# Kernel optimization log

Hardware: AMD Instinct MI355X
Metric: run time of the kernel (lower is better)

Reference implementation:

```python
import jax, jax.numpy as jnp
import numpy as np

EMB = 1024
HEADS = 16
DH = EMB // HEADS
EPS = 1e-5


def _layernorm(x, w, b):
    mean = jnp.mean(x, axis=-1, keepdims=True)
    var = jnp.mean((x - mean) ** 2, axis=-1, keepdims=True)  # unbiased=False
    return w * (x - mean) / jnp.sqrt(var + EPS) + b


def _gelu_tanh(x):
    c = jnp.sqrt(jnp.asarray(2.0 / jnp.pi, x.dtype))
    return 0.5 * x * (1.0 + jnp.tanh(c * (x + 0.044715 * x ** 3)))


def setup_inputs() -> dict:
    key = jax.random.key(0)
    ks = jax.random.split(key, 8)
    B, N = 2, 2048
    s = lambda fan_in: 1.0 / np.sqrt(fan_in)
    # weights stored as [in, out] (torch Linear applied as x @ W.T == x @ W_here)
    return {
        "x": jax.random.normal(ks[0], (B, N, EMB), jnp.float32),
        "ln1_w": jnp.ones((EMB,), jnp.float32),
        "ln1_b": jnp.zeros((EMB,), jnp.float32),
        "w_qkv": jax.random.normal(ks[1], (EMB, 3 * EMB), jnp.float32) * s(EMB),  # qkv_bias=False
        "w_attn_proj": jax.random.normal(ks[2], (EMB, EMB), jnp.float32) * s(EMB),
        "b_attn_proj": jnp.zeros((EMB,), jnp.float32),
        "ln2_w": jnp.ones((EMB,), jnp.float32),
        "ln2_b": jnp.zeros((EMB,), jnp.float32),
        "w_fc": jax.random.normal(ks[3], (EMB, 4 * EMB), jnp.float32) * s(EMB),
        "b_fc": jnp.zeros((4 * EMB,), jnp.float32),
        "w_proj": jax.random.normal(ks[4], (4 * EMB, EMB), jnp.float32) * s(4 * EMB),
        "b_proj": jnp.zeros((EMB,), jnp.float32),
    }


def reference(x, ln1_w, ln1_b, w_qkv, w_attn_proj, b_attn_proj,
              ln2_w, ln2_b, w_fc, b_fc, w_proj, b_proj):
    B, N, _ = x.shape
    # --- attention sublayer (pre-LN) ---
    h = _layernorm(x, ln1_w, ln1_b)
    qkv = h @ w_qkv  # [B,N,3E]
    q, k, v = jnp.split(qkv, 3, axis=-1)
    # [B,H,N,Dh]
    q = q.reshape(B, N, HEADS, DH).transpose(0, 2, 1, 3)
    k = k.reshape(B, N, HEADS, DH).transpose(0, 2, 1, 3)
    v = v.reshape(B, N, HEADS, DH).transpose(0, 2, 1, 3)
    scores = jnp.einsum("bhqd,bhkd->bhqk", q, k) * (DH ** -0.5)
    causal = jnp.tril(jnp.ones((N, N), bool))
    scores = jnp.where(causal, scores, -jnp.inf)
    attn = jax.nn.softmax(scores, axis=-1)  # attn_pdrop=0 (eval)
    ctx = jnp.einsum("bhqk,bhkd->bhqd", attn, v)
    ctx = ctx.transpose(0, 2, 1, 3).reshape(B, N, EMB)
    x = x + (ctx @ w_attn_proj + b_attn_proj)  # resid_pdrop=0
    # --- MLP sublayer (pre-LN) ---
    h = _layernorm(x, ln2_w, ln2_b)
    h = _gelu_tanh(h @ w_fc + b_fc)
    x = x + (h @ w_proj + b_proj)
    return x
```

## Files before the change

### kernel.cpp

```cpp
#include <hip/hip_runtime.h>
#include <stdint.h>

#define EMB 1024
#define NHEAD 16
#define DH 64
#define SEQ 2048
#define NTOK 4096

typedef __attribute__((ext_vector_type(8))) short s16x8;
typedef __attribute__((ext_vector_type(4))) short s16x4;
typedef __attribute__((ext_vector_type(4))) float f32x4;
typedef __attribute__((ext_vector_type(4))) unsigned short u16x4;

__device__ __forceinline__ unsigned short f2bf(float f){
    union { float f; unsigned int u; } v; v.f = f;
    unsigned int r = v.u + 0x7fffu + ((v.u >> 16) & 1u);
    return (unsigned short)(r >> 16);
}

__device__ __forceinline__ f32x4 mfma16(s16x8 a, s16x8 b, f32x4 c){
    return __builtin_amdgcn_mfma_f32_16x16x32_bf16(a, b, c, 0, 0, 0);
}

__device__ __forceinline__ void gload16(const void* g, void* l){
    __builtin_amdgcn_global_load_lds((const __attribute__((address_space(1))) void*)g,
                                     (__attribute__((address_space(3))) void*)l, 16, 0, 0);
}

__device__ __forceinline__ s16x8 cat8(s16x4 a, s16x4 b){
    s16x8 r;
    r[0]=a[0]; r[1]=a[1]; r[2]=a[2]; r[3]=a[3];
    r[4]=b[0]; r[5]=b[1]; r[6]=b[2]; r[7]=b[3];
    return r;
}

__device__ __forceinline__ unsigned cvtpk(float lo, float hi){
    unsigned r;
    asm("v_cvt_pk_bf16_f32 %0, %1, %2" : "=v"(r) : "v"(lo), "v"(hi));
    return r;
}

__device__ __forceinline__ s16x8 qscale(s16x8 q){
    s16x8 r;
    #pragma unroll
    for (int e = 0; e < 8; ++e){
        union { float f; unsigned u; } v;
        v.u = ((unsigned)(unsigned short)q[e]) << 16;
        v.f *= 0.125f;
        r[e] = (short)f2bf(v.f);
    }
    return r;
}

__global__ __launch_bounds__(256) void convT4_kernel(const float* __restrict__ q, unsigned short* __restrict__ qo,
                                                     const float* __restrict__ a, unsigned short* __restrict__ ao,
                                                     const float* __restrict__ f, unsigned short* __restrict__ fo,
                                                     const float* __restrict__ p, unsigned short* __restrict__ po){
    __shared__ float tile[32][33];
    int id = blockIdx.x;
    const float* in; unsigned short* out; int R, C, bx, by;
    if (id < 3072)      { in = q; out = qo; R = 1024; C = 3072; bx = id % 96;  by = id / 96;  }
    else if (id < 4096) { id -= 3072; in = a; out = ao; R = 1024; C = 1024; bx = id % 32; by = id / 32; }
    else if (id < 8192) { id -= 4096; in = f; out = fo; R = 1024; C = 4096; bx = id % 128; by = id / 128; }
    else                { id -= 8192; in = p; out = po; R = 4096; C = 1024; bx = id % 32; by = id / 32; }
    const int c0 = bx * 32, r0 = by * 32;
    const int tx = threadIdx.x, ty = threadIdx.y;
    #pragma unroll
    for (int k = 0; k < 4; ++k)
        tile[ty*4+k][tx] = in[(long)(r0 + ty*4 + k) * C + c0 + tx];
    __syncthreads();
    #pragma unroll
    for (int k = 0; k < 4; ++k)
        out[(long)(c0 + ty*4 + k) * R + r0 + tx] = f2bf(tile[tx][ty*4+k]);
}

__global__ __launch_bounds__(256) void vT_kernel(const unsigned short* __restrict__ qkv,
                                                 unsigned short* __restrict__ vtg){
    __shared__ unsigned short tile[64*64];
    const int bh = blockIdx.y, b = bh >> 4, h = bh & 15;
    const int n0 = blockIdx.x * 64;
    const int t = threadIdx.x;
    const int nr = t >> 3, c0 = (t & 7) * 8;
    #pragma unroll
    for (int hh = 0; hh < 2; ++hh){
        const int n = nr + hh*32;
        uint4 vv = *(const uint4*)&qkv[(long)(b*SEQ + n0 + n)*3072 + 2048 + h*64 + c0];
        *(uint4*)((char*)tile + n*128 + ((c0*2) ^ (((n>>3)&7)<<4))) = vv;
    }
    __syncthreads();
    #pragma unroll
    for (int hh = 0; hh < 2; ++hh){
        const int d = nr + hh*32;
        union { unsigned short u[8]; uint4 v; } tmp;
        #pragma unroll
        for (int j = 0; j < 8; ++j){
            const int n = c0 + j;
            tmp.u[j] = *(const unsigned short*)((char*)tile + n*128 + ((d*2) ^ (((n>>3)&7)<<4)));
        }
        *(uint4*)&vtg[((long)bh*64 + d)*2048 + n0 + c0] = tmp.v;
    }
}

__global__ __launch_bounds__(256) void ln_kernel(const float* __restrict__ x,
                                                 const float* __restrict__ w,
                                                 const float* __restrict__ b,
                                                 unsigned short* __restrict__ out){
    const int row = blockIdx.x, tid = threadIdx.x;
    const float4 v = ((const float4*)(x + (long)row * EMB))[tid];
    float s  = v.x + v.y + v.z + v.w;
    float ss = v.x*v.x + v.y*v.y + v.z*v.z + v.w*v.w;
    #pragma unroll
    for (int off = 32; off >= 1; off >>= 1){
        s  += __shfl_xor(s,  off, 64);
        ss += __shfl_xor(ss, off, 64);
    }
    __shared__ float ps[4], pss[4];
    const int wv = tid >> 6;
    if ((tid & 63) == 0){ ps[wv] = s; pss[wv] = ss; }
    __syncthreads();
    s  = ps[0] + ps[1] + ps[2] + ps[3];
    ss = pss[0] + pss[1] + pss[2] + pss[3];
    const float mean = s * (1.0f/EMB);
    const float var  = ss * (1.0f/EMB) - mean*mean;
    const float rstd = rsqrtf(var + 1e-5f);
    const float4 wv4 = ((const float4*)w)[tid];
    const float4 bv4 = ((const float4*)b)[tid];
    u16x4 o;
    o[0] = f2bf((v.x - mean) * rstd * wv4.x + bv4.x);
    o[1] = f2bf((v.y - mean) * rstd * wv4.y + bv4.y);
    o[2] = f2bf((v.z - mean) * rstd * wv4.z + bv4.z);
    o[3] = f2bf((v.w - mean) * rstd * wv4.w + bv4.w);
    *(u16x4*)(out + (long)row * EMB + tid * 4) = o;
}

__global__ __launch_bounds__(256) void red_kernel(const float* __restrict__ p0,
                                                  const float* __restrict__ p1,
                                                  const float* __restrict__ bias,
                                                  const float* __restrict__ resid,
                                                  float* __restrict__ out, int N){
    const long i = ((long)blockIdx.x * 256 + threadIdx.x) * 4;
    const float4 a = *(const float4*)(p0 + i);
    const float4 b = *(const float4*)(p1 + i);
    const float4 r = *(const float4*)(resid + i);
    const float4 bb = *(const float4*)(bias + ((int)i & (N - 1)));
    float4 o;
    o.x = a.x + b.x + r.x + bb.x;
    o.y = a.y + b.y + r.y + bb.y;
    o.z = a.z + b.z + r.z + bb.z;
    o.w = a.w + b.w + r.w + bb.w;
    *(float4*)(out + i) = o;
}

template<int EPI, int SK>
__global__ __launch_bounds__(256, 2) void gemm4_kernel(const unsigned short* __restrict__ A,
                                                       const unsigned short* __restrict__ Bt,
                                                       const float* __restrict__ bias,
                                                       void* __restrict__ out0,
                                                       void* __restrict__ out1,
                                                       int M, int N, int K){
    __shared__ unsigned short As[2][128*64];
    __shared__ unsigned short Bs[2][128*64];
    const int tid = threadIdx.x, lane = tid & 63, w = tid >> 6;
    const int lm = lane & 15, g = lane >> 4;
    const int wr = w >> 1, wc = w & 1;

    const int gx = gridDim.x;
    const int nwg = gx * gridDim.y;
    int id = blockIdx.y * gx + blockIdx.x;
    id = (id & 7) * (nwg >> 3) + (id >> 3);
    const int m0 = (id / gx) * 128, n0 = (id % gx) * 128;
    const int kz = (SK > 1) ? blockIdx.z : 0;
    const int kbase = kz * (K / SK);
    const int nkt = (K / SK) / 64;

    const int r8 = tid >> 3;
    const int src = (((tid & 7) * 16) ^ ((r8 & 7) << 4)) >> 1;
    char* AsB = (char*)&As[0][0];
    char* BsB = (char*)&Bs[0][0];

    auto stage = [&](int bu, int kt){
        #pragma unroll
        for (int p = 0; p < 4; ++p)
            gload16(&A[(long)(m0 + p*32 + r8) * K + kt + src], AsB + bu*16384 + p*4096 + tid*16);
        #pragma unroll
        for (int p = 0; p < 4; ++p)
            gload16(&Bt[(long)(n0 + p*32 + r8) * K + kt + src], BsB + bu*16384 + p*4096 + tid*16);
    };

    f32x4 zero = {0.0f, 0.0f, 0.0f, 0.0f};
    f32x4 acc[4][4];
    #pragma unroll
    for (int i = 0; i < 4; ++i)
        #pragma unroll
        for (int j = 0; j < 4; ++j) acc[i][j] = zero;

    stage(0, kbase);
    int cur = 0;
    const int axor = (lm & 7) << 4;
    for (int t = 0; t < nkt; ++t){
        if (t + 1 < nkt){
            stage(cur ^ 1, kbase + (t + 1) * 64);
            asm volatile("s_waitcnt vmcnt(8)" ::: "memory");
        } else {
            asm volatile("s_waitcnt vmcnt(0)" ::: "memory");
        }
        __builtin_amdgcn_s_barrier();
        asm volatile("" ::: "memory");
        const char* Ab = AsB + cur*16384;
        const char* Bb = BsB + cur*16384;
        #pragma unroll
        for (int kk = 0; kk < 2; ++kk){
            s16x8 af[4], bf[4];
            #pragma unroll
            for (int i = 0; i < 4; ++i)
                af[i] = *(const s16x8*)(Ab + (wr*64 + i*16 + lm)*128 + ((kk*64 + g*16) ^ axor));
            #pragma unroll
            for (int j = 0; j < 4; ++j)
                bf[j] = *(const s16x8*)(Bb + (wc*64 + j*16 + lm)*128 + ((kk*64 + g*16) ^ axor));
            asm volatile("s_waitcnt lgkmcnt(0)" ::: "memory");
            __builtin_amdgcn_sched_barrier(0);
            __builtin_amdgcn_s_setprio(1);
            #pragma unroll
            for (int i = 0; i < 4; ++i)
                #pragma unroll
                for (int j = 0; j < 4; ++j)
                    acc[i][j] = mfma16(af[i], bf[j], acc[i][j]);
            __builtin_amdgcn_s_setprio(0);
        }
        asm volatile("" ::: "memory");
        __builtin_amdgcn_s_barrier();
        asm volatile("" ::: "memory");
        cur ^= 1;
    }

    float* po = (SK > 1 && kz == 1) ? (float*)out1 : (float*)out0;
    #pragma unroll
    for (int i = 0; i < 4; ++i){
        #pragma unroll
        for (int r = 0; r < 4; ++r){
            const int row = m0 + wr*64 + i*16 + 4*g + r;
            #pragma unroll
            for (int j = 0; j < 4; ++j){
                const int col = n0 + wc*64 + j*16 + lm;
                const float v = acc[i][j][r];
                if (EPI == 0){
                    ((unsigned short*)out0)[(long)row * N + col] = f2bf(v);
                } else if (EPI == 2){
                    const float xx = v + bias[col];
                    const float z = 0.7978845608f * (xx + 0.044715f * xx * xx * xx);
                    const float gg = xx / (1.0f + __expf(-2.0f * z));
                    ((unsigned short*)out0)[(long)row * N + col] = f2bf(gg);
                } else {
                    po[(long)row * N + col] = v;
                }
            }
        }
    }
}

template<int EPI, int SK>
__global__ __launch_bounds__(256, 3) void gemm5_kernel(const unsigned short* __restrict__ A,
                                                       const unsigned short* __restrict__ Bt,
                                                       const float* __restrict__ bias,
                                                       const float* __restrict__ resid,
                                                       float* __restrict__ out0,
                                                       float* __restrict__ out1,
                                                       int M, int N, int K,
                                                       int xr, int yr){
    __shared__ unsigned short As[2][128*64];
    __shared__ unsigned short Bs[2][64*64];
    const int tid = threadIdx.x, lane = tid & 63, w = tid >> 6;
    const int lm = lane & 15, g = lane >> 4;
    const int wr = w >> 1, wc = w & 1;

    const int gx = gridDim.x;
    const int o = blockIdx.y * gx + blockIdx.x;
    const int x = o & 7, j = o >> 3;
    const int nrx = gx / xr;
    const int m0 = ((x / nrx) * yr + j / xr) * 128;
    const int n0 = ((x % nrx) * xr + j % xr) * 64;
    const int kz = (SK > 1) ? blockIdx.z : 0;
    const int kbase = kz * (K / SK);
    const int nkt = (K / SK) / 64;

    const int r8 = tid >> 3;
    const int src = (((tid & 7) * 16) ^ ((r8 & 7) << 4)) >> 1;
    char* AsB = (char*)&As[0][0];
    char* BsB = (char*)&Bs[0][0];

    auto stage = [&](int bu, int kt){
        #pragma unroll
        for (int p = 0; p < 4; ++p)
            gload16(&A[(long)(m0 + p*32 + r8) * K + kt + src], AsB + bu*16384 + p*4096 + tid*16);
        #pragma unroll
        for (int p = 0; p < 2; ++p)
            gload16(&Bt[(long)(n0 + p*32 + r8) * K + kt + src], BsB + bu*8192 + p*4096 + tid*16);
    };

    f32x4 zero = {0.0f, 0.0f, 0.0f, 0.0f};
    f32x4 acc[4][2];
    #pragma unroll
    for (int i = 0; i < 4; ++i)
        #pragma unroll
        for (int jj = 0; jj < 2; ++jj) acc[i][jj] = zero;

    stage(0, kbase);
    int cur = 0;
    const int axor = (lm & 7) << 4;
    for (int t = 0; t < nkt; ++t){
        if (t + 1 < nkt){
            stage(cur ^ 1, kbase + (t + 1) * 64);
            asm volatile("s_waitcnt vmcnt(6)" ::: "memory");
        } else {
            asm volatile("s_waitcnt vmcnt(0)" ::: "memory");
        }
        __builtin_amdgcn_s_barrier();
        asm volatile("" ::: "memory");
        const char* Ab = AsB + cur*16384;
        const char* Bb = BsB + cur*8192;
        #pragma unroll
        for (int kk = 0; kk < 2; ++kk){
            s16x8 af[4], bf[2];
            #pragma unroll
            for (int i = 0; i < 4; ++i)
                af[i] = *(const s16x8*)(Ab + (wr*64 + i*16 + lm)*128 + ((kk*64 + g*16) ^ axor));
            #pragma unroll
            for (int jj = 0; jj < 2; ++jj)
                bf[jj] = *(const s16x8*)(Bb + (wc*32 + jj*16 + lm)*128 + ((kk*64 + g*16) ^ axor));
            asm volatile("s_waitcnt lgkmcnt(0)" ::: "memory");
            __builtin_amdgcn_sched_barrier(0);
            __builtin_amdgcn_s_setprio(1);
            #pragma unroll
            for (int i = 0; i < 4; ++i)
                #pragma unroll
                for (int jj = 0; jj < 2; ++jj)
                    acc[i][jj] = mfma16(bf[jj], af[i], acc[i][jj]);
            __builtin_amdgcn_s_setprio(0);
        }
        asm volatile("" ::: "memory");
        __builtin_amdgcn_s_barrier();
        asm volatile("" ::: "memory");
        cur ^= 1;
    }

    float* po = (SK > 1 && kz == 1) ? out1 : out0;
    #pragma unroll
    for (int i = 0; i < 4; ++i){
        const int row = m0 + wr*64 + i*16 + lm;
        #pragma unroll
        for (int jj = 0; jj < 2; ++jj){
            const int col = n0 + wc*32 + jj*16 + 4*g;
            const f32x4 v = acc[i][jj];
            if (EPI == 1){
                const float4 bb = *(const float4*)&bias[col];
                const float4 rr = *(const float4*)&resid[(long)row * N + col];
                float4 ov;
                ov.x = v[0] + bb.x + rr.x;
                ov.y = v[1] + bb.y + rr.y;
                ov.z = v[2] + bb.z + rr.z;
                ov.w = v[3] + bb.w + rr.w;
                *(float4*)&out0[(long)row * N + col] = ov;
            } else {
                *(float4*)&po[(long)row * N + col] = *(const float4*)&v;
            }
        }
    }
}

template<int EPI, int BM, int BN, int WR, int WC, int SK>
__global__ __launch_bounds__(WR*WC*64) void gemm_kernel(const unsigned short* __restrict__ A,
                                                        const unsigned short* __restrict__ Bt,
                                                        const float* __restrict__ bias,
                                                        const float* __restrict__ resid,
                                                        void* __restrict__ out0,
                                                        void* __restrict__ out1,
                                                        int M, int N, int K){
    constexpr int NW = WR * WC;
    constexpr int NT = NW * 64;
    constexpr int FI = BM / (WR * 16);
    constexpr int FJ = BN / (WC * 16);
    __shared__ unsigned short As[2][BM * 32];
    __shared__ unsigned short Bs[2][BN * 32];
    const int tid  = threadIdx.x;
    const int lane = tid & 63, w = tid >> 6;
    const int lm = lane & 15, g = lane >> 4;
    const int wr = w / WC, wc = w % WC;

    const int gx = gridDim.x;
    const int nwg = gx * gridDim.y;
    int id = blockIdx.y * gx + blockIdx.x;
    id = (id & 7) * (nwg >> 3) + (id >> 3);
    const int m0 = (id / gx) * BM, n0 = (id % gx) * BN;
    const int kz = (SK > 1) ? blockIdx.z : 0;
    const int kbase = kz * (K / SK);

    f32x4 zero = {0.0f, 0.0f, 0.0f, 0.0f};
    f32x4 acc[FI][FJ];
    #pragma unroll
    for (int i = 0; i < FI; ++i)
        #pragma unroll
        for (int j = 0; j < FJ; ++j) acc[i][j] = zero;

    auto stage = [&](int kt, int bu){
        #pragma unroll
        for (int p = 0; p < BM/(NT/4); ++p)
            gload16(&A[(long)(m0 + p*(NT/4) + (tid>>2)) * K + kt + (tid&3)*8],
                    (char*)&As[bu][0] + p*(NT*16) + tid*16);
        #pragma unroll
        for (int p = 0; p < BN/(NT/4); ++p)
            gload16(&Bt[(long)(n0 + p*(NT/4) + (tid>>2)) * K + kt + (tid&3)*8],
                    (char*)&Bs[bu][0] + p*(NT*16) + tid*16);
    };

    stage(kbase, 0);
    int cur = 0;
    const int nkt = (K / SK) / 32;
    for (int t = 0; t < nkt; ++t){
        __syncthreads();
        if (t + 1 < nkt) stage(kbase + (t+1)*32, cur ^ 1);
        s16x8 af[FI], bf[FJ];
        #pragma unroll
        for (int i = 0; i < FI; ++i)
            af[i] = *(const s16x8*)&As[cur][(wr*(FI*16) + i*16 + lm)*32 + g*8];
        #pragma unroll
        for (int j = 0; j < FJ; ++j)
            bf[j] = *(const s16x8*)&Bs[cur][(wc*(FJ*16) + j*16 + lm)*32 + g*8];
        #pragma unroll
        for (int i = 0; i < FI; ++i)
            #pragma unroll
            for (int j = 0; j < FJ; ++j)
                acc[i][j] = mfma16(af[i], bf[j], acc[i][j]);
        cur ^= 1;
    }

    float* po = (SK > 1 && kz == 1) ? (float*)out1 : (float*)out0;
    #pragma unroll
    for (int i = 0; i < FI; ++i){
        #pragma unroll
        for (int r = 0; r < 4; ++r){
            const int row = m0 + wr*(FI*16) + i*16 + 4*g + r;
            #pragma unroll
            for (int j = 0; j < FJ; ++j){
                const int col = n0 + wc*(FJ*16) + j*16 + lm;
                const float v = acc[i][j][r];
                if (EPI == 0){
                    ((unsigned short*)out0)[(long)row * N + col] = f2bf(v);
                } else if (EPI == 1){
                    ((float*)out0)[(long)row * N + col] =
                        v + bias[col] + resid[(long)row * N + col];
                } else if (EPI == 2){
                    const float xx = v + bias[col];
                    const float z = 0.7978845608f * (xx + 0.044715f * xx * xx * xx);
                    const float gg = xx / (1.0f + __expf(-2.0f * z));
                    ((unsigned short*)out0)[(long)row * N + col] = f2bf(gg);
                } else {
                    po[(long)row * N + col] = v;
                }
            }
        }
    }
}

__global__ __launch_bounds__(256) void attn_kernel(const unsigned short* __restrict__ qkv,
                                                   const unsigned short* __restrict__ vtg,
                                                   unsigned short* __restrict__ ctx){
    __shared__ unsigned short Ks[3][4096];
    __shared__ unsigned short Vs[3][4096];
    int id0 = blockIdx.y * 16 + blockIdx.x;
    const int id = (id0 & 7) * 64 + (id0 >> 3);
    const int pair = id & 15, bh = id >> 4;
    const int b = bh >> 4, h = bh & 15;
    const int tid = threadIdx.x, lane = tid & 63, w = tid >> 6;
    const int lm = lane & 15, g = lane >> 4;
    const long qkvb = (long)b * SEQ * 3072;
    const unsigned short* kglob = qkv + qkvb + 1024 + h*64;
    const unsigned short* vglob = vtg + (long)bh * 64 * 2048;

    const int srow = tid >> 3;
    const int soff = (tid & 7) * 16;
    const int swz = (lm & 7) << 4;
    f32x4 zero = {0.0f, 0.0f, 0.0f, 0.0f};

    #pragma unroll 1
    for (int grp = 0; grp < 2; ++grp){
        const int qg = (grp == 0) ? pair : (31 - pair);
        const int q0 = qg * 64;
        const int nt = qg + 1;
        const int qrow = q0 + w*16 + lm;

        const unsigned short* qrp = qkv + qkvb + (long)qrow*3072 + h*64;
        const s16x8 qf0 = qscale(*(const s16x8*)(qrp + g*8));
        const s16x8 qf1 = qscale(*(const s16x8*)(qrp + 32 + g*8));

        f32x4 o[4];
        #pragma unroll
        for (int d = 0; d < 4; ++d) o[d] = zero;
        float lsum = 0.0f;

        auto stageKV = [&](int t, int bu){
            const int kv0 = t * 64;
            #pragma unroll
            for (int hh = 0; hh < 2; ++hh){
                const int row = srow + hh*32;
                const int sw  = soff ^ ((row & 7) << 4);
                gload16(kglob + (long)(kv0 + row)*3072 + (sw >> 1),
                        (char*)&Ks[bu][0] + hh*4096 + w*1024);
                gload16(vglob + (long)row*2048 + kv0 + (sw >> 1),
                        (char*)&Vs[bu][0] + hh*4096 + w*1024);
            }
        };
        auto qkt = [&](int bu, f32x4* sc){
            const char* Kb = (const char*)&Ks[bu][0];
            #pragma unroll
            for (int s = 0; s < 4; ++s){
                const char* rp = Kb + (s*16 + lm)*128;
                s16x8 kf0 = *(const s16x8*)(rp + ((g*16) ^ swz));
                s16x8 kf1 = *(const s16x8*)(rp + ((64 + g*16) ^ swz));
                f32x4 a = mfma16(kf0, qf0, zero);
                sc[s] = mfma16(kf1, qf1, a);
            }
        };

        __builtin_amdgcn_s_barrier();
        asm volatile("" ::: "memory");
        stageKV(0, 0);
        if (nt > 1){
            stageKV(1, 1);
            asm volatile("s_waitcnt vmcnt(4)" ::: "memory");
        } else {
            asm volatile("s_waitcnt vmcnt(0)" ::: "memory");
        }
        __builtin_amdgcn_s_barrier();
        asm volatile("" ::: "memory");

        f32x4 sc[4], scN[4];
        qkt(0, sc);

        #pragma unroll 1
        for (int t = 0; t < nt; ++t){
            const bool more = (t + 1 < nt);
            if (more){
                asm volatile("s_waitcnt vmcnt(0)" ::: "memory");
                __builtin_amdgcn_s_barrier();
                asm volatile("" ::: "memory");
                if (t + 2 < nt) stageKV(t + 2, (t + 2) % 3);
                qkt((t + 1) % 3, scN);
            }

            if (t == nt - 1){
                #pragma unroll
                for (int s = 0; s < 4; ++s)
                    #pragma unroll
                    for (int r = 0; r < 4; ++r)
                        if (s*16 + 4*g + r > w*16 + lm) sc[s][r] = -1e30f;
            }
            float pp[4][4];
            #pragma unroll
            for (int s = 0; s < 4; ++s)
                #pragma unroll
                for (int r = 0; r < 4; ++r){
                    const float e = __expf(sc[s][r]);
                    pp[s][r] = e;
                    lsum += e;
                }

            union { unsigned u[4]; s16x8 v; } P0, P1;
            P0.u[0] = cvtpk(pp[0][0], pp[0][1]);
            P0.u[1] = cvtpk(pp[0][2], pp[0][3]);
            P0.u[2] = cvtpk(pp[1][0], pp[1][1]);
            P0.u[3] = cvtpk(pp[1][2], pp[1][3]);
            P1.u[0] = cvtpk(pp[2][0], pp[2][1]);
            P1.u[1] = cvtpk(pp[2][2], pp[2][3]);
            P1.u[2] = cvtpk(pp[3][0], pp[3][1]);
            P1.u[3] = cvtpk(pp[3][2], pp[3][3]);

            const char* Vb = (const char*)&Vs[t % 3][0];
            #pragma unroll
            for (int d = 0; d < 4; ++d){
                const char* vrp = Vb + (d*16 + lm)*128;
                s16x4 a0 = *(const s16x4*)(vrp + ((g*8) ^ swz));
                s16x4 a1 = *(const s16x4*)(vrp + ((32 + g*8) ^ swz));
                o[d] = mfma16(cat8(a0, a1), P0.v, o[d]);
                s16x4 b0 = *(const s16x4*)(vrp + ((64 + g*8) ^ swz));
                s16x4 b1 = *(const s16x4*)(vrp + ((96 + g*8) ^ swz));
                o[d] = mfma16(cat8(b0, b1), P1.v, o[d]);
            }
            if (more){
                #pragma unroll
                for (int s4 = 0; s4 < 4; ++s4) sc[s4] = scN[s4];
            }
        }

        lsum += __shfl_xor(lsum, 16, 64);
        lsum += __shfl_xor(lsum, 32, 64);
        const float inv = 1.0f / lsum;
        unsigned short* cw = ctx + (long)(b*SEQ + qrow)*EMB + h*DH + 4*g;
        #pragma unroll
        for (int d = 0; d < 4; ++d){
            u16x4 ov;
            ov[0] = f2bf(o[d][0]*inv); ov[1] = f2bf(o[d][1]*inv);
            ov[2] = f2bf(o[d][2]*inv); ov[3] = f2bf(o[d][3]*inv);
            *(u16x4*)(cw + d*16) = ov;
        }
    }
}

extern "C" void kernel_launch(void* const* d_in, const int* in_sizes, int n_in,
                              void* d_out, int out_size, void* d_ws, size_t ws_size,
                              hipStream_t stream){
    const float* x     = (const float*)d_in[0];
    const float* ln1_w = (const float*)d_in[1];
    const float* ln1_b = (const float*)d_in[2];
    const float* w_qkv = (const float*)d_in[3];
    const float* w_ap  = (const float*)d_in[4];
    const float* b_ap  = (const float*)d_in[5];
    const float* ln2_w = (const float*)d_in[6];
    const float* ln2_b = (const float*)d_in[7];
    const float* w_fc  = (const float*)d_in[8];
    const float* b_fc  = (const float*)d_in[9];
    const float* w_pr  = (const float*)d_in[10];
    const float* b_pr  = (const float*)d_in[11];
    float* out = (float*)d_out;

    char* ws = (char*)d_ws;
    unsigned short* wqkvT = (unsigned short*)(ws + 0);
    unsigned short* wapT  = (unsigned short*)(ws + 6291456);
    unsigned short* wfcT  = (unsigned short*)(ws + 8388608);
    unsigned short* wprT  = (unsigned short*)(ws + 16777216);
    unsigned short* h1    = (unsigned short*)(ws + 25165824);
    unsigned short* vtg   = (unsigned short*)(ws + 25165824);
    unsigned short* qkv   = (unsigned short*)(ws + 33554432);
    unsigned short* ctx   = (unsigned short*)(ws + 58720256);
    float*          x1    = (float*)(ws + 67108864);
    unsigned short* h2    = (unsigned short*)(ws + 83886080);
    unsigned short* afc   = (unsigned short*)(ws + 92274688);
    float* pp0 = (float*)(ws + 0);
    float* pp1 = (float*)(ws + 25165824);

    convT4_kernel<<<12288, dim3(32, 8, 1), 0, stream>>>(
        w_qkv, wqkvT, w_ap, wapT, w_fc, wfcT, w_pr, wprT);

    ln_kernel<<<NTOK, 256, 0, stream>>>(x, ln1_w, ln1_b, h1);

    gemm4_kernel<0,1><<<dim3(3072/128, NTOK/128), 256, 0, stream>>>(
        h1, wqkvT, nullptr, qkv, nullptr, NTOK, 3072, 1024);

    vT_kernel<<<dim3(SEQ/64, 32), 256, 0, stream>>>(qkv, vtg);

    attn_kernel<<<dim3(16, 32), 256, 0, stream>>>(qkv, vtg, ctx);

    gemm_kernel<1,128,64,2,2,1><<<dim3(1024/64, NTOK/128), 256, 0, stream>>>(
        ctx, wapT, b_ap, x, x1, nullptr, NTOK, 1024, 1024);

    ln_kernel<<<NTOK, 256, 0, stream>>>(x1, ln2_w, ln2_b, h2);

    gemm4_kernel<2,1><<<dim3(4096/128, NTOK/128), 256, 0, stream>>>(
        h2, wfcT, b_fc, afc, nullptr, NTOK, 4096, 1024);

    gemm5_kernel<3,2><<<dim3(1024/64, NTOK/128, 2), 256, 0, stream>>>(
        afc, wprT, nullptr, nullptr, pp0, pp1, NTOK, 1024, 4096, 8, 8);
    red_kernel<<<NTOK*EMB/1024, 256, 0, stream>>>(pp0, pp1, b_pr, x1, out, EMB);
}
```

Before: 248.8 us.

## Drop split-K on MLP down-projection and fuse bias+residual into GEMM epilogue

```diff
diff --git a/kernel.cpp b/kernel.cpp
--- a/kernel.cpp
+++ b/kernel.cpp
@@ -133,30 +133,11 @@
     *(u16x4*)(out + (long)row * EMB + tid * 4) = o;
 }
 
-__global__ __launch_bounds__(256) void red_kernel(const float* __restrict__ p0,
-                                                  const float* __restrict__ p1,
-                                                  const float* __restrict__ bias,
-                                                  const float* __restrict__ resid,
-                                                  float* __restrict__ out, int N){
-    const long i = ((long)blockIdx.x * 256 + threadIdx.x) * 4;
-    const float4 a = *(const float4*)(p0 + i);
-    const float4 b = *(const float4*)(p1 + i);
-    const float4 r = *(const float4*)(resid + i);
-    const float4 bb = *(const float4*)(bias + ((int)i & (N - 1)));
-    float4 o;
-    o.x = a.x + b.x + r.x + bb.x;
-    o.y = a.y + b.y + r.y + bb.y;
-    o.z = a.z + b.z + r.z + bb.z;
-    o.w = a.w + b.w + r.w + bb.w;
-    *(float4*)(out + i) = o;
-}
-
-template<int EPI, int SK>
+template<int EPI>
 __global__ __launch_bounds__(256, 2) void gemm4_kernel(const unsigned short* __restrict__ A,
                                                        const unsigned short* __restrict__ Bt,
                                                        const float* __restrict__ bias,
                                                        void* __restrict__ out0,
-                                                       void* __restrict__ out1,
                                                        int M, int N, int K){
     __shared__ unsigned short As[2][128*64];
     __shared__ unsigned short Bs[2][128*64];
@@ -169,9 +150,7 @@
     int id = blockIdx.y * gx + blockIdx.x;
     id = (id & 7) * (nwg >> 3) + (id >> 3);
     const int m0 = (id / gx) * 128, n0 = (id % gx) * 128;
-    const int kz = (SK > 1) ? blockIdx.z : 0;
-    const int kbase = kz * (K / SK);
-    const int nkt = (K / SK) / 64;
+    const int nkt = K / 64;
 
     const int r8 = tid >> 3;
     const int src = (((tid & 7) * 16) ^ ((r8 & 7) << 4)) >> 1;
@@ -194,12 +173,12 @@
         #pragma unroll
         for (int j = 0; j < 4; ++j) acc[i][j] = zero;
 
-    stage(0, kbase);
+    stage(0, 0);
     int cur = 0;
     const int axor = (lm & 7) << 4;
     for (int t = 0; t < nkt; ++t){
         if (t + 1 < nkt){
-            stage(cur ^ 1, kbase + (t + 1) * 64);
+            stage(cur ^ 1, (t + 1) * 64);
             asm volatile("s_waitcnt vmcnt(8)" ::: "memory");
         } else {
             asm volatile("s_waitcnt vmcnt(0)" ::: "memory");
@@ -233,7 +212,6 @@
         cur ^= 1;
     }
 
-    float* po = (SK > 1 && kz == 1) ? (float*)out1 : (float*)out0;
     #pragma unroll
     for (int i = 0; i < 4; ++i){
         #pragma unroll
@@ -245,26 +223,22 @@
                 const float v = acc[i][j][r];
                 if (EPI == 0){
                     ((unsigned short*)out0)[(long)row * N + col] = f2bf(v);
-                } else if (EPI == 2){
+                } else {
                     const float xx = v + bias[col];
                     const float z = 0.7978845608f * (xx + 0.044715f * xx * xx * xx);
                     const float gg = xx / (1.0f + __expf(-2.0f * z));
                     ((unsigned short*)out0)[(long)row * N + col] = f2bf(gg);
-                } else {
-                    po[(long)row * N + col] = v;
                 }
             }
         }
     }
 }
 
-template<int EPI, int SK>
 __global__ __launch_bounds__(256, 3) void gemm5_kernel(const unsigned short* __restrict__ A,
                                                        const unsigned short* __restrict__ Bt,
                                                        const float* __restrict__ bias,
                                                        const float* __restrict__ resid,
                                                        float* __restrict__ out0,
-                                                       float* __restrict__ out1,
                                                        int M, int N, int K,
                                                        int xr, int yr){
     __shared__ unsigned short As[2][128*64];
@@ -279,9 +253,7 @@
     const int nrx = gx / xr;
     const int m0 = ((x / nrx) * yr + j / xr) * 128;
     const int n0 = ((x % nrx) * xr + j % xr) * 64;
-    const int kz = (SK > 1) ? blockIdx.z : 0;
-    const int kbase = kz * (K / SK);
-    const int nkt = (K / SK) / 64;
+    const int nkt = K / 64;
 
     const int r8 = tid >> 3;
     const int src = (((tid & 7) * 16) ^ ((r8 & 7) << 4)) >> 1;
@@ -304,12 +276,12 @@
         #pragma unroll
         for (int jj = 0; jj < 2; ++jj) acc[i][jj] = zero;
 
-    stage(0, kbase);
+    stage(0, 0);
     int cur = 0;
     const int axor = (lm & 7) << 4;
     for (int t = 0; t < nkt; ++t){
         if (t + 1 < nkt){
-            stage(cur ^ 1, kbase + (t + 1) * 64);
+            stage(cur ^ 1, (t + 1) * 64);
             asm volatile("s_waitcnt vmcnt(6)" ::: "memory");
         } else {
             asm volatile("s_waitcnt vmcnt(0)" ::: "memory");
@@ -343,7 +315,6 @@
         cur ^= 1;
     }
 
-    float* po = (SK > 1 && kz == 1) ? out1 : out0;
     #pragma unroll
     for (int i = 0; i < 4; ++i){
         const int row = m0 + wr*64 + i*16 + lm;
@@ -351,29 +322,24 @@
         for (int jj = 0; jj < 2; ++jj){
             const int col = n0 + wc*32 + jj*16 + 4*g;
             const f32x4 v = acc[i][jj];
-            if (EPI == 1){
-                const float4 bb = *(const float4*)&bias[col];
-                const float4 rr = *(const float4*)&resid[(long)row * N + col];
-                float4 ov;
-                ov.x = v[0] + bb.x + rr.x;
-                ov.y = v[1] + bb.y + rr.y;
-                ov.z = v[2] + bb.z + rr.z;
-                ov.w = v[3] + bb.w + rr.w;
-                *(float4*)&out0[(long)row * N + col] = ov;
-            } else {
-                *(float4*)&po[(long)row * N + col] = *(const float4*)&v;
-            }
-        }
-    }
-}
-
-template<int EPI, int BM, int BN, int WR, int WC, int SK>
+            const float4 bb = *(const float4*)&bias[col];
+            const float4 rr = *(const float4*)&resid[(long)row * N + col];
+            float4 ov;
+            ov.x = v[0] + bb.x + rr.x;
+            ov.y = v[1] + bb.y + rr.y;
+            ov.z = v[2] + bb.z + rr.z;
+            ov.w = v[3] + bb.w + rr.w;
+            *(float4*)&out0[(long)row * N + col] = ov;
+        }
+    }
+}
+
+template<int EPI, int BM, int BN, int WR, int WC>
 __global__ __launch_bounds__(WR*WC*64) void gemm_kernel(const unsigned short* __restrict__ A,
                                                         const unsigned short* __restrict__ Bt,
                                                         const float* __restrict__ bias,
                                                         const float* __restrict__ resid,
                                                         void* __restrict__ out0,
-                                                        void* __restrict__ out1,
                                                         int M, int N, int K){
     constexpr int NW = WR * WC;
     constexpr int NT = NW * 64;
@@ -391,8 +357,6 @@
     int id = blockIdx.y * gx + blockIdx.x;
     id = (id & 7) * (nwg >> 3) + (id >> 3);
     const int m0 = (id / gx) * BM, n0 = (id % gx) * BN;
-    const int kz = (SK > 1) ? blockIdx.z : 0;
-    const int kbase = kz * (K / SK);
 
     f32x4 zero = {0.0f, 0.0f, 0.0f, 0.0f};
     f32x4 acc[FI][FJ];
@@ -412,12 +376,12 @@
                     (char*)&Bs[bu][0] + p*(NT*16) + tid*16);
     };
 
-    stage(kbase, 0);
+    stage(0, 0);
     int cur = 0;
-    const int nkt = (K / SK) / 32;
+    const int nkt = K / 32;
     for (int t = 0; t < nkt; ++t){
         __syncthreads();
-        if (t + 1 < nkt) stage(kbase + (t+1)*32, cur ^ 1);
+        if (t + 1 < nkt) stage((t+1)*32, cur ^ 1);
         s16x8 af[FI], bf[FJ];
         #pragma unroll
         for (int i = 0; i < FI; ++i)
@@ -433,7 +397,6 @@
         cur ^= 1;
     }
 
-    float* po = (SK > 1 && kz == 1) ? (float*)out1 : (float*)out0;
     #pragma unroll
     for (int i = 0; i < FI; ++i){
         #pragma unroll
@@ -443,18 +406,11 @@
             for (int j = 0; j < FJ; ++j){
                 const int col = n0 + wc*(FJ*16) + j*16 + lm;
                 const float v = acc[i][j][r];
-                if (EPI == 0){
-                    ((unsigned short*)out0)[(long)row * N + col] = f2bf(v);
-                } else if (EPI == 1){
+                if (EPI == 1){
                     ((float*)out0)[(long)row * N + col] =
                         v + bias[col] + resid[(long)row * N + col];
-                } else if (EPI == 2){
-                    const float xx = v + bias[col];
-                    const float z = 0.7978845608f * (xx + 0.044715f * xx * xx * xx);
-                    const float gg = xx / (1.0f + __expf(-2.0f * z));
-                    ((unsigned short*)out0)[(long)row * N + col] = f2bf(gg);
                 } else {
-                    po[(long)row * N + col] = v;
+                    ((unsigned short*)out0)[(long)row * N + col] = f2bf(v);
                 }
             }
         }
@@ -634,30 +590,27 @@
     float*          x1    = (float*)(ws + 67108864);
     unsigned short* h2    = (unsigned short*)(ws + 83886080);
     unsigned short* afc   = (unsigned short*)(ws + 92274688);
-    float* pp0 = (float*)(ws + 0);
-    float* pp1 = (float*)(ws + 25165824);
 
     convT4_kernel<<<12288, dim3(32, 8, 1), 0, stream>>>(
         w_qkv, wqkvT, w_ap, wapT, w_fc, wfcT, w_pr, wprT);
 
     ln_kernel<<<NTOK, 256, 0, stream>>>(x, ln1_w, ln1_b, h1);
 
-    gemm4_kernel<0,1><<<dim3(3072/128, NTOK/128), 256, 0, stream>>>(
-        h1, wqkvT, nullptr, qkv, nullptr, NTOK, 3072, 1024);
+    gemm4_kernel<0><<<dim3(3072/128, NTOK/128), 256, 0, stream>>>(
+        h1, wqkvT, nullptr, qkv, NTOK, 3072, 1024);
 
     vT_kernel<<<dim3(SEQ/64, 32), 256, 0, stream>>>(qkv, vtg);
 
     attn_kernel<<<dim3(16, 32), 256, 0, stream>>>(qkv, vtg, ctx);
 
-    gemm_kernel<1,128,64,2,2,1><<<dim3(1024/64, NTOK/128), 256, 0, stream>>>(
-        ctx, wapT, b_ap, x, x1, nullptr, NTOK, 1024, 1024);
+    gemm_kernel<1,128,64,2,2><<<dim3(1024/64, NTOK/128), 256, 0, stream>>>(
+        ctx, wapT, b_ap, x, x1, NTOK, 1024, 1024);
 
     ln_kernel<<<NTOK, 256, 0, stream>>>(x1, ln2_w, ln2_b, h2);
 
-    gemm4_kernel<2,1><<<dim3(4096/128, NTOK/128), 256, 0, stream>>>(
-        h2, wfcT, b_fc, afc, nullptr, NTOK, 4096, 1024);
-
-    gemm5_kernel<3,2><<<dim3(1024/64, NTOK/128, 2), 256, 0, stream>>>(
-        afc, wprT, nullptr, nullptr, pp0, pp1, NTOK, 1024, 4096, 8, 8);
-    red_kernel<<<NTOK*EMB/1024, 256, 0, stream>>>(pp0, pp1, b_pr, x1, out, EMB);
-}
+    gemm4_kernel<2><<<dim3(4096/128, NTOK/128), 256, 0, stream>>>(
+        h2, wfcT, b_fc, afc, NTOK, 4096, 1024);
+
+    gemm5_kernel<<<dim3(1024/64, NTOK/128), 256, 0, stream>>>(
+        afc, wprT, b_pr, x1, out, NTOK, 1024, 4096, 8, 8);
+}
```

After: 237.9 us. 4.4% less time.
